# Kernel optimization log

Hardware: AMD Instinct MI355X
Metric: run time of the kernel (lower is better)

Reference implementation:

```python
import jax, jax.numpy as jnp
import numpy as np

N_NODES = 100000
N_EDGES = 1000000
D_FEAT = 64
THR_LO, THR_HI = 0.6, 0.8
LOG_CLAMP = -100.0  # torch BCELoss clamps log terms at -100


def setup_inputs() -> dict:
    key = jax.random.key(0)
    k1, k2, k3 = jax.random.split(key, 3)
    edges_nn = jax.random.randint(k1, (N_EDGES, 2), 0, N_NODES, dtype=jnp.int64)
    probas = jax.random.uniform(k2, (N_NODES,), dtype=jnp.float32)
    feats = jax.random.normal(k3, (N_NODES, D_FEAT), dtype=jnp.float32)
    return {"edges_nn": edges_nn, "probas": probas, "feats": feats}


def reference(edges_nn, probas, feats):
    # Per-edge endpoint probabilities. [E]
    pi = probas[edges_nn[:, 0]]
    pj = probas[edges_nn[:, 1]]

    # Similar edges: both endpoints confidently positive (label 1).
    mask_sim = (pi >= THR_HI) & (pj >= THR_HI)
    # Dissimilar edges: one confident positive, the other confident negative (label 0).
    mask_disim = ((pi >= THR_HI) & (pj < THR_LO)) | ((pj >= THR_HI) & (pi < THR_LO))

    # Gather endpoint features and compute pairwise L2 distance for ALL edges
    # (masked afterwards; avoids dynamic shapes, stays jit-friendly). [E, D] -> [E]
    diff = feats[edges_nn[:, 0]] - feats[edges_nn[:, 1]]
    d = jnp.sqrt(jnp.sum(diff * diff, axis=1))
    p = jnp.exp(-d)  # predicted similarity in (0, 1]

    # BCE per edge (torch-style log clamping at -100).
    #   sim   (target 1): -log(p)   = d (clamped)
    #   disim (target 0): -log(1-p)
    bce_sim = -jnp.maximum(jnp.log(p), LOG_CLAMP)
    bce_disim = -jnp.maximum(jnp.log1p(-p), LOG_CLAMP)

    n_sim = jnp.sum(mask_sim).astype(jnp.float32)
    n_disim = jnp.sum(mask_disim).astype(jnp.float32)
    total = n_sim + n_disim

    # Class-balancing weights from the original: sim edges weighted by the
    # fraction of disim edges and vice versa.
    pos_weight = n_disim / total
    neg_weight = n_sim / total

    sim_sum = jnp.sum(jnp.where(mask_sim, bce_sim, 0.0))
    disim_sum = jnp.sum(jnp.where(mask_disim, bce_disim, 0.0))

    loss = (sim_sum * pos_weight + disim_sum * neg_weight) / total
    return loss
```

## Files before the change

kernel.cpp:

```cpp
#include <hip/hip_runtime.h>
#include <math.h>

#define N_EDGES   1000000
#define THR_LO    0.6f
#define THR_HI    0.8f
#define LOG_CLAMP -100.0f

#define NBLOCKS   2048
#define BLOCK     256


__global__ void __launch_bounds__(BLOCK)
edge_loss_kernel(const int2* __restrict__ edges,
                 const float* __restrict__ probas,
                 const float4* __restrict__ feats,
                 float4* __restrict__ part) {
    int tid    = blockIdx.x * blockDim.x + threadIdx.x;
    int stride = gridDim.x * blockDim.x;

    float sim = 0.f, disim = 0.f, ns = 0.f, nd = 0.f;

    for (int e = tid; e < N_EDGES; e += stride) {
        int2 ij = edges[e];
        float pi = probas[ij.x];
        float pj = probas[ij.y];
        bool msim = (pi >= THR_HI) & (pj >= THR_HI);
        bool mdis = ((pi >= THR_HI) & (pj < THR_LO)) |
                    ((pj >= THR_HI) & (pi < THR_LO));
        if (msim | mdis) {
            const float4* fi = feats + (size_t)ij.x * 16;
            const float4* fj = feats + (size_t)ij.y * 16;
            float s = 0.f;
            #pragma unroll
            for (int k = 0; k < 16; ++k) {
                float4 a = fi[k];
                float4 b = fj[k];
                float dx = a.x - b.x, dy = a.y - b.y;
                float dz = a.z - b.z, dw = a.w - b.w;
                s += dx * dx + dy * dy + dz * dz + dw * dw;
            }
            float d = sqrtf(s);
            if (msim) {
                sim += fminf(d, 100.0f);
                ns  += 1.0f;
            }
            if (mdis) {
                float p = expf(-d);
                disim += -fmaxf(log1pf(-p), LOG_CLAMP);
                nd    += 1.0f;
            }
        }
    }

    #pragma unroll
    for (int off = 32; off > 0; off >>= 1) {
        sim   += __shfl_down(sim,   off);
        disim += __shfl_down(disim, off);
        ns    += __shfl_down(ns,    off);
        nd    += __shfl_down(nd,    off);
    }

    __shared__ float lds[4][4];
    int lane = threadIdx.x & 63;
    int wave = threadIdx.x >> 6;
    if (lane == 0) {
        lds[wave][0] = sim;
        lds[wave][1] = disim;
        lds[wave][2] = ns;
        lds[wave][3] = nd;
    }
    __syncthreads();
    if (threadIdx.x == 0) {
        float a = 0.f, b = 0.f, c = 0.f, d4 = 0.f;
        #pragma unroll
        for (int w = 0; w < 4; ++w) {
            a  += lds[w][0];
            b  += lds[w][1];
            c  += lds[w][2];
            d4 += lds[w][3];
        }
        part[blockIdx.x] = make_float4(a, b, c, d4);
    }
}

__global__ void __launch_bounds__(BLOCK)
finalize_kernel(const float4* __restrict__ part,
                float* __restrict__ out) {
    float a = 0.f, b = 0.f, c = 0.f, d4 = 0.f;
    for (int i = threadIdx.x; i < NBLOCKS; i += BLOCK) {
        float4 p = part[i];
        a += p.x; b += p.y; c += p.z; d4 += p.w;
    }
    #pragma unroll
    for (int off = 32; off > 0; off >>= 1) {
        a  += __shfl_down(a,  off);
        b  += __shfl_down(b,  off);
        c  += __shfl_down(c,  off);
        d4 += __shfl_down(d4, off);
    }
    __shared__ float lds[4][4];
    int lane = threadIdx.x & 63;
    int wave = threadIdx.x >> 6;
    if (lane == 0) {
        lds[wave][0] = a; lds[wave][1] = b; lds[wave][2] = c; lds[wave][3] = d4;
    }
    __syncthreads();
    if (threadIdx.x == 0) {
        float sim_sum = 0.f, disim_sum = 0.f, n_sim = 0.f, n_disim = 0.f;
        #pragma unroll
        for (int w = 0; w < 4; ++w) {
            sim_sum   += lds[w][0];
            disim_sum += lds[w][1];
            n_sim     += lds[w][2];
            n_disim   += lds[w][3];
        }
        float total = n_sim + n_disim;
        out[0] = (sim_sum * (n_disim / total) +
                  disim_sum * (n_sim / total)) / total;
    }
}

extern "C" void kernel_launch(void* const* d_in, const int* in_sizes, int n_in,
                              void* d_out, int out_size, void* d_ws, size_t ws_size,
                              hipStream_t stream) {
    const int*   edges  = (const int*)d_in[0];
    const float* probas = (const float*)d_in[1];
    const float* feats  = (const float*)d_in[2];
    float4* part = (float4*)d_ws;

    edge_loss_kernel<<<NBLOCKS, BLOCK, 0, stream>>>(
        (const int2*)edges, probas, (const float4*)feats, part);

    finalize_kernel<<<1, BLOCK, 0, stream>>>(part, (float*)d_out);
}
```

Before: 107.0 us.

## Compact active edges per wave and gather features cooperatively with 4-lane groups

Each wave ballots which edges pass the similarity/dissimilarity masks, compacts their endpoint indices into LDS, and then has groups of 4 lanes split each 64-float feature row, so the feature gathers are coalesced and divergence is removed. Each group handles two edges per iteration to raise memory-level parallelism, and edge counts come from popcounts. This aims to avoid the per-thread divergent 256-byte row reads of the sparse surviving edges. It adds block-level syncs, LDS traffic and shuffle reductions.

```diff
diff --git a/kernel.cpp b/kernel.cpp
--- a/kernel.cpp
+++ b/kernel.cpp
@@ -10,74 +10,124 @@
 #define BLOCK     256
 
 
+__device__ __forceinline__ void accum_edge(float s, int simflag,
+                                           float& sim, float& dis) {
+    float d = sqrtf(s);
+    if (simflag) {
+        sim += fminf(d, 100.0f);
+    } else {
+        float p = expf(-d);
+        dis += -fmaxf(log1pf(-p), LOG_CLAMP);
+    }
+}
+
 __global__ void __launch_bounds__(BLOCK)
 edge_loss_kernel(const int2* __restrict__ edges,
                  const float* __restrict__ probas,
                  const float4* __restrict__ feats,
                  float4* __restrict__ part) {
-    int tid    = blockIdx.x * blockDim.x + threadIdx.x;
-    int stride = gridDim.x * blockDim.x;
+    const int lane = threadIdx.x & 63;
+    const int wave = threadIdx.x >> 6;
+    const int grp  = lane >> 2;
+    const int sub  = lane & 3;
 
-    float sim = 0.f, disim = 0.f, ns = 0.f, nd = 0.f;
+    __shared__ int sh_i[4][64];
+    __shared__ int sh_j[4][64];
 
-    for (int e = tid; e < N_EDGES; e += stride) {
-        int2 ij = edges[e];
+    float sim = 0.f, dis = 0.f, ns = 0.f, nd = 0.f;
+
+    const int gstride = gridDim.x * blockDim.x;
+    for (int base = blockIdx.x * blockDim.x; base < N_EDGES; base += gstride) {
+        int e = base + threadIdx.x;
+        bool in = (e < N_EDGES);
+        int2 ij = in ? edges[e] : make_int2(0, 0);
         float pi = probas[ij.x];
         float pj = probas[ij.y];
-        bool msim = (pi >= THR_HI) & (pj >= THR_HI);
-        bool mdis = ((pi >= THR_HI) & (pj < THR_LO)) |
-                    ((pj >= THR_HI) & (pi < THR_LO));
+        bool msim = in & (pi >= THR_HI) & (pj >= THR_HI);
+        bool mdis = in & (((pi >= THR_HI) & (pj < THR_LO)) |
+                          ((pj >= THR_HI) & (pi < THR_LO)));
+
+        unsigned long long balsim = __ballot(msim);
+        unsigned long long baldis = __ballot(mdis);
+        unsigned long long m      = balsim | baldis;
+        if (lane == 0) {
+            ns += (float)__popcll(balsim);
+            nd += (float)__popcll(baldis);
+        }
+        int count = __popcll(m);
+
         if (msim | mdis) {
-            const float4* fi = feats + (size_t)ij.x * 16;
-            const float4* fj = feats + (size_t)ij.y * 16;
-            float s = 0.f;
-            #pragma unroll
-            for (int k = 0; k < 16; ++k) {
-                float4 a = fi[k];
-                float4 b = fj[k];
-                float dx = a.x - b.x, dy = a.y - b.y;
-                float dz = a.z - b.z, dw = a.w - b.w;
-                s += dx * dx + dy * dy + dz * dz + dw * dw;
-            }
-            float d = sqrtf(s);
-            if (msim) {
-                sim += fminf(d, 100.0f);
-                ns  += 1.0f;
-            }
-            if (mdis) {
-                float p = expf(-d);
-                disim += -fmaxf(log1pf(-p), LOG_CLAMP);
-                nd    += 1.0f;
+            int prefix = __popcll(m & ((1ULL << lane) - 1ULL));
+            sh_i[wave][prefix] = ij.x | (msim ? (int)0x80000000 : 0);
+            sh_j[wave][prefix] = ij.y;
+        }
+        __syncthreads();
+
+        for (int t = grp; t < count; t += 32) {
+            bool h2 = (t + 16) < count;
+            int  tb = h2 ? t + 16 : t;
+
+            int xa_i = sh_i[wave][t],  xa_j = sh_j[wave][t];
+            int xb_i = sh_i[wave][tb], xb_j = sh_j[wave][tb];
+
+            const float4* rai = feats + (size_t)(xa_i & 0x7FFFFFFF) * 16;
+            const float4* raj = feats + (size_t)xa_j * 16;
+            const float4* rbi = feats + (size_t)(xb_i & 0x7FFFFFFF) * 16;
+            const float4* rbj = feats + (size_t)xb_j * 16;
+
+            float4 A0 = rai[sub], A1 = rai[sub + 4], A2 = rai[sub + 8], A3 = rai[sub + 12];
+            float4 B0 = raj[sub], B1 = raj[sub + 4], B2 = raj[sub + 8], B3 = raj[sub + 12];
+            float4 C0 = rbi[sub], C1 = rbi[sub + 4], C2 = rbi[sub + 8], C3 = rbi[sub + 12];
+            float4 D0 = rbj[sub], D1 = rbj[sub + 4], D2 = rbj[sub + 8], D3 = rbj[sub + 12];
+
+            float s1 = 0.f, s2 = 0.f, dx, dy, dz, dw;
+            dx = A0.x-B0.x; dy = A0.y-B0.y; dz = A0.z-B0.z; dw = A0.w-B0.w;
+            s1 += dx*dx + dy*dy + dz*dz + dw*dw;
+            dx = A1.x-B1.x; dy = A1.y-B1.y; dz = A1.z-B1.z; dw = A1.w-B1.w;
+            s1 += dx*dx + dy*dy + dz*dz + dw*dw;
+            dx = A2.x-B2.x; dy = A2.y-B2.y; dz = A2.z-B2.z; dw = A2.w-B2.w;
+            s1 += dx*dx + dy*dy + dz*dz + dw*dw;
+            dx = A3.x-B3.x; dy = A3.y-B3.y; dz = A3.z-B3.z; dw = A3.w-B3.w;
+            s1 += dx*dx + dy*dy + dz*dz + dw*dw;
+
+            dx = C0.x-D0.x; dy = C0.y-D0.y; dz = C0.z-D0.z; dw = C0.w-D0.w;
+            s2 += dx*dx + dy*dy + dz*dz + dw*dw;
+            dx = C1.x-D1.x; dy = C1.y-D1.y; dz = C1.z-D1.z; dw = C1.w-D1.w;
+            s2 += dx*dx + dy*dy + dz*dz + dw*dw;
+            dx = C2.x-D2.x; dy = C2.y-D2.y; dz = C2.z-D2.z; dw = C2.w-D2.w;
+            s2 += dx*dx + dy*dy + dz*dz + dw*dw;
+            dx = C3.x-D3.x; dy = C3.y-D3.y; dz = C3.z-D3.z; dw = C3.w-D3.w;
+            s2 += dx*dx + dy*dy + dz*dz + dw*dw;
+
+            s1 += __shfl_xor(s1, 1); s1 += __shfl_xor(s1, 2);
+            s2 += __shfl_xor(s2, 1); s2 += __shfl_xor(s2, 2);
+
+            if (sub == 0) {
+                accum_edge(s1, ((unsigned)xa_i) >> 31, sim, dis);
+                if (h2) accum_edge(s2, ((unsigned)xb_i) >> 31, sim, dis);
             }
         }
+        __syncthreads();
     }
 
     #pragma unroll
     for (int off = 32; off > 0; off >>= 1) {
-        sim   += __shfl_down(sim,   off);
-        disim += __shfl_down(disim, off);
-        ns    += __shfl_down(ns,    off);
-        nd    += __shfl_down(nd,    off);
+        sim += __shfl_down(sim, off);
+        dis += __shfl_down(dis, off);
+        ns  += __shfl_down(ns,  off);
+        nd  += __shfl_down(nd,  off);
     }
-
     __shared__ float lds[4][4];
-    int lane = threadIdx.x & 63;
-    int wave = threadIdx.x >> 6;
     if (lane == 0) {
-        lds[wave][0] = sim;
-        lds[wave][1] = disim;
-        lds[wave][2] = ns;
-        lds[wave][3] = nd;
+        lds[wave][0] = sim; lds[wave][1] = dis;
+        lds[wave][2] = ns;  lds[wave][3] = nd;
     }
     __syncthreads();
     if (threadIdx.x == 0) {
         float a = 0.f, b = 0.f, c = 0.f, d4 = 0.f;
         #pragma unroll
         for (int w = 0; w < 4; ++w) {
-            a  += lds[w][0];
-            b  += lds[w][1];
-            c  += lds[w][2];
-            d4 += lds[w][3];
+            a += lds[w][0]; b += lds[w][1]; c += lds[w][2]; d4 += lds[w][3];
         }
         part[blockIdx.x] = make_float4(a, b, c, d4);
     }
```

Result: faster. 99.66 us (-6.9%).
